# Performance work log

Measured on AMD Instinct MI355X. Metric: run time of the kernel, lower is better.

## Reference

```python
import jax, jax.numpy as jnp
import numpy as np

D_MODEL = 2048
N_HEADS = 16
HEAD_DIM = D_MODEL // N_HEADS  # 128
B, T = 2, 2048


def setup_inputs() -> dict:
    key = jax.random.key(0)
    ks = jax.random.split(key, 5)
    s = 0.02
    x = jax.random.normal(ks[0], (B, T, D_MODEL), dtype=jnp.float32)
    # weights stored as [in, out] (math-equivalent to torch Linear's W.T)
    Wq = jax.random.normal(ks[1], (D_MODEL, D_MODEL), dtype=jnp.float32) * s
    Wk = jax.random.normal(ks[2], (D_MODEL, HEAD_DIM), dtype=jnp.float32) * s
    Wv = jax.random.normal(ks[3], (D_MODEL, HEAD_DIM), dtype=jnp.float32) * s
    Wo = jax.random.normal(ks[4], (D_MODEL, D_MODEL), dtype=jnp.float32) * s
    return {"x": x, "Wq": Wq, "Wk": Wk, "Wv": Wv, "Wo": Wo}


def reference(x, Wq, Wk, Wv, Wo):
    Bx, Tx, Dx = x.shape
    scale = HEAD_DIM ** -0.5
    # q: (B, H, T, hd); k, v: single shared head (B, T, hd)
    q = (x @ Wq).reshape(Bx, Tx, N_HEADS, HEAD_DIM).transpose(0, 2, 1, 3)
    k = x @ Wk  # (B, T, hd)
    v = x @ Wv  # (B, T, hd)
    # scores: (B, H, T, T) -- shared KV head broadcast across query heads
    attn = jnp.einsum('bhqd,bkd->bhqk', q, k) * scale
    causal = jnp.triu(jnp.ones((Tx, Tx), dtype=bool), k=1)  # True = masked
    attn = jnp.where(causal[None, None], -jnp.inf, attn)
    weights = jax.nn.softmax(attn, axis=-1)
    weights = jnp.nan_to_num(weights)
    out = jnp.einsum('bhqk,bkd->bhqd', weights, v)  # (B, H, T, hd)
    out = out.transpose(0, 2, 1, 3).reshape(Bx, Tx, Dx)
    return out @ Wo
```

## Files before the change

### kernel.cpp

```cpp
#include <hip/hip_runtime.h>

typedef __bf16 bf16x8 __attribute__((ext_vector_type(8)));
typedef float f32x4 __attribute__((ext_vector_type(4)));

__device__ inline void gload16(const __bf16* g, __bf16* l) {
  __builtin_amdgcn_global_load_lds(
      (const __attribute__((address_space(1))) unsigned int*)g,
      (__attribute__((address_space(3))) unsigned int*)l, 16, 0, 0);
}

__global__ __launch_bounds__(256) void conv_bf16(
    const float* __restrict__ in, __bf16* __restrict__ out)
{
  size_t i = ((size_t)blockIdx.x * 256 + threadIdx.x) * 8;
  float4 a = *(const float4*)&in[i];
  float4 b = *(const float4*)&in[i + 4];
  bf16x8 h;
  h[0] = (__bf16)a.x; h[1] = (__bf16)a.y; h[2] = (__bf16)a.z; h[3] = (__bf16)a.w;
  h[4] = (__bf16)b.x; h[5] = (__bf16)b.y; h[6] = (__bf16)b.z; h[7] = (__bf16)b.w;
  *(bf16x8*)&out[i] = h;
}

__global__ __launch_bounds__(256) void transpose_w(
    const float* __restrict__ W, __bf16* __restrict__ WT, int Kd, int Nd)
{
  __shared__ __bf16 Ts[64 * 72];
  const int tid = threadIdx.x;
  const int c0 = blockIdx.x * 64, r0 = blockIdx.y * 64;
#pragma unroll
  for (int i = 0; i < 4; i++) {
    int row = (tid >> 4) + i * 16, cv = (tid & 15) * 4;
    float4 w = *(const float4*)&W[(size_t)(r0 + row) * Nd + c0 + cv];
    Ts[(cv + 0) * 72 + row] = (__bf16)w.x;
    Ts[(cv + 1) * 72 + row] = (__bf16)w.y;
    Ts[(cv + 2) * 72 + row] = (__bf16)w.z;
    Ts[(cv + 3) * 72 + row] = (__bf16)w.w;
  }
  __syncthreads();
#pragma unroll
  for (int i = 0; i < 4; i++) {
    int n = (tid >> 4) + i * 16, kseg = (tid & 15) * 4;
    *(uint2*)&WT[(size_t)(c0 + n) * Kd + r0 + kseg] = *(uint2*)&Ts[n * 72 + kseg];
  }
}

__global__ __launch_bounds__(256) void gemm_qkv(
    const __bf16* __restrict__ A, const __bf16* __restrict__ WqT,
    const __bf16* __restrict__ WkT, const __bf16* __restrict__ WvT,
    __bf16* __restrict__ Cq, __bf16* __restrict__ Ck, __bf16* __restrict__ Cv)
{
  __shared__ __align__(16) __bf16 Asl[128 * 32];
  __shared__ __align__(16) __bf16 Bsl[128 * 32];
  const int tid = threadIdx.x, wave = tid >> 6, lane = tid & 63;
  const int quad = lane >> 4, l16 = lane & 15;
  const int nb = blockIdx.x, m0 = blockIdx.y * 128;
  const __bf16* BT; __bf16* C; int ldC, c0;
  if (nb < 16)       { BT = WqT + (size_t)nb * 128 * 2048; C = Cq; ldC = 2048; c0 = nb * 128; }
  else if (nb == 16) { BT = WkT; C = Ck; ldC = 128; c0 = 0; }
  else               { BT = WvT; C = Cv; ldC = 128; c0 = 0; }
  const int wm = (wave >> 1) * 64, wn = (wave & 1) * 64;
  const int lrow = lane >> 2, lseg = (lane & 3) * 8;

  f32x4 acc[4][4];
#pragma unroll
  for (int i = 0; i < 4; i++)
#pragma unroll
    for (int j = 0; j < 4; j++) acc[i][j] = (f32x4){0.f, 0.f, 0.f, 0.f};

  for (int k0 = 0; k0 < 2048; k0 += 32) {
    __syncthreads();
#pragma unroll
    for (int c = 0; c < 2; c++) {
      int ch = wave * 2 + c;
      gload16(&A[(size_t)(m0 + ch * 16 + lrow) * 2048 + k0 + lseg], &Asl[ch * 512]);
      gload16(&BT[(size_t)(ch * 16 + lrow) * 2048 + k0 + lseg], &Bsl[ch * 512]);
    }
    __syncthreads();

    bf16x8 af[4], bf[4];
#pragma unroll
    for (int i = 0; i < 4; i++)
      af[i] = *(const bf16x8*)&Asl[(wm + i * 16 + l16) * 32 + quad * 8];
#pragma unroll
    for (int i = 0; i < 4; i++)
      bf[i] = *(const bf16x8*)&Bsl[(wn + i * 16 + l16) * 32 + quad * 8];
#pragma unroll
    for (int mi = 0; mi < 4; mi++)
#pragma unroll
      for (int ni = 0; ni < 4; ni++)
        acc[mi][ni] = __builtin_amdgcn_mfma_f32_16x16x32_bf16(
            af[mi], bf[ni], acc[mi][ni], 0, 0, 0);
  }

#pragma unroll
  for (int mi = 0; mi < 4; mi++)
#pragma unroll
    for (int ni = 0; ni < 4; ni++)
#pragma unroll
      for (int r = 0; r < 4; r++) {
        int row = m0 + wm + mi * 16 + quad * 4 + r;
        int col = c0 + wn + ni * 16 + l16;
        C[(size_t)row * ldC + col] = (__bf16)acc[mi][ni][r];
      }
}

__global__ __launch_bounds__(256) void gemm_out_bt(
    const __bf16* __restrict__ A, const __bf16* __restrict__ BT,
    float* __restrict__ Cp)
{
  __shared__ __align__(16) __bf16 Asl[128 * 32];
  __shared__ __align__(16) __bf16 Bsl[128 * 32];
  const int tid = threadIdx.x, wave = tid >> 6, lane = tid & 63;
  const int quad = lane >> 4, l16 = lane & 15;
  const int n0 = blockIdx.x * 128, m0 = blockIdx.y * 128;
  const int wm = (wave >> 1) * 64, wn = (wave & 1) * 64;
  const int lrow = lane >> 2, lseg = (lane & 3) * 8;

  f32x4 acc[4][4];
#pragma unroll
  for (int i = 0; i < 4; i++)
#pragma unroll
    for (int j = 0; j < 4; j++) acc[i][j] = (f32x4){0.f, 0.f, 0.f, 0.f};

  for (int k0 = 0; k0 < 2048; k0 += 32) {
    __syncthreads();
#pragma unroll
    for (int c = 0; c < 2; c++) {
      int ch = wave * 2 + c;
      gload16(&A[(size_t)(m0 + ch * 16 + lrow) * 2048 + k0 + lseg], &Asl[ch * 512]);
      gload16(&BT[(size_t)(n0 + ch * 16 + lrow) * 2048 + k0 + lseg], &Bsl[ch * 512]);
    }
    __syncthreads();

    bf16x8 af[4], bf[4];
#pragma unroll
    for (int i = 0; i < 4; i++)
      af[i] = *(const bf16x8*)&Asl[(wm + i * 16 + l16) * 32 + quad * 8];
#pragma unroll
    for (int i = 0; i < 4; i++)
      bf[i] = *(const bf16x8*)&Bsl[(wn + i * 16 + l16) * 32 + quad * 8];
#pragma unroll
    for (int mi = 0; mi < 4; mi++)
#pragma unroll
      for (int ni = 0; ni < 4; ni++)
        acc[mi][ni] = __builtin_amdgcn_mfma_f32_16x16x32_bf16(
            af[mi], bf[ni], acc[mi][ni], 0, 0, 0);
  }

#pragma unroll
  for (int mi = 0; mi < 4; mi++)
#pragma unroll
    for (int ni = 0; ni < 4; ni++)
#pragma unroll
      for (int r = 0; r < 4; r++) {
        int row = m0 + wm + mi * 16 + quad * 4 + r;
        int col = n0 + wn + ni * 16 + l16;
        Cp[(size_t)row * 2048 + col] = acc[mi][ni][r];
      }
}

__global__ __launch_bounds__(256) void gemm_out_f32b(
    const __bf16* __restrict__ A, const float* __restrict__ B,
    float* __restrict__ Cp)
{
  __shared__ __align__(16) __bf16 Asl[128 * 32];
  __shared__ __align__(16) __bf16 BsT[128 * 32];
  const int tid = threadIdx.x, wave = tid >> 6, lane = tid & 63;
  const int quad = lane >> 4, l16 = lane & 15;
  const int n0 = blockIdx.x * 128, m0 = blockIdx.y * 128;
  const int wm = (wave >> 1) * 64, wn = (wave & 1) * 64;
  const int lrow = lane >> 2, lseg = (lane & 3) * 8;
  const int kg = (tid >> 5) * 4, ng = (tid & 31) * 4;

  f32x4 acc[4][4];
#pragma unroll
  for (int i = 0; i < 4; i++)
#pragma unroll
    for (int j = 0; j < 4; j++) acc[i][j] = (f32x4){0.f, 0.f, 0.f, 0.f};

  for (int k0 = 0; k0 < 2048; k0 += 32) {
    __syncthreads();
#pragma unroll
    for (int c = 0; c < 2; c++) {
      int ch = wave * 2 + c;
      gload16(&A[(size_t)(m0 + ch * 16 + lrow) * 2048 + k0 + lseg], &Asl[ch * 512]);
    }
    __bf16 h[4][4];
#pragma unroll
    for (int i = 0; i < 4; i++) {
      float4 w = *(const float4*)&B[(size_t)(k0 + kg + i) * 2048 + n0 + ng];
      h[i][0] = (__bf16)w.x; h[i][1] = (__bf16)w.y;
      h[i][2] = (__bf16)w.z; h[i][3] = (__bf16)w.w;
    }
#pragma unroll
    for (int j = 0; j < 4; j++) {
      int n = ng + j;
      int pb = ((kg >> 3) + (n >> 2)) & 3;
      __bf16 o4[4] = {h[0][j], h[1][j], h[2][j], h[3][j]};
      *(uint2*)&BsT[n * 32 + pb * 8 + (kg & 7)] = *(uint2*)o4;
    }
    __syncthreads();

    bf16x8 af[4], bf[4];
#pragma unroll
    for (int i = 0; i < 4; i++)
      af[i] = *(const bf16x8*)&Asl[(wm + i * 16 + l16) * 32 + quad * 8];
#pragma unroll
    for (int i = 0; i < 4; i++) {
      int n = wn + i * 16 + l16;
      int pb = (quad + (n >> 2)) & 3;
      bf[i] = *(const bf16x8*)&BsT[n * 32 + pb * 8];
    }
#pragma unroll
    for (int mi = 0; mi < 4; mi++)
#pragma unroll
      for (int ni = 0; ni < 4; ni++)
        acc[mi][ni] = __builtin_amdgcn_mfma_f32_16x16x32_bf16(
            af[mi], bf[ni], acc[mi][ni], 0, 0, 0);
  }

#pragma unroll
  for (int mi = 0; mi < 4; mi++)
#pragma unroll
    for (int ni = 0; ni < 4; ni++)
#pragma unroll
      for (int r = 0; r < 4; r++) {
        int row = m0 + wm + mi * 16 + quad * 4 + r;
        int col = n0 + wn + ni * 16 + l16;
        Cp[(size_t)row * 2048 + col] = acc[mi][ni][r];
      }
}

#define KS_LD 136
#define VT_LD 72
#define PR_LD 72

__global__ __launch_bounds__(256) void mqa_attn_mfma(
    const __bf16* Q, const __bf16* __restrict__ Km,
    const __bf16* __restrict__ Vm, __bf16* O)
{
  __shared__ __align__(16) __bf16 Ks[64 * KS_LD];
  __shared__ __align__(16) __bf16 VsT[128 * VT_LD];
  __shared__ __align__(16) __bf16 Pr[4][32 * PR_LD];

  const int tid = threadIdx.x, wave = tid >> 6, lane = tid & 63;
  const int quad = lane >> 4, l16 = lane & 15;
  const int t = blockIdx.x >> 1, bat = blockIdx.x & 1;
  const int hg = blockIdx.y & 3, flip = blockIdx.y >> 2;
  const int qt = flip ? (63 - t) : t;
  const int h = hg * 4 + wave;
  const int q0 = qt * 32;
  const size_t qgrow = (size_t)bat * 2048 + q0;
  const float SCL2 = 0.08838834764831845f * 1.4426950408889634f;

  bf16x8 qf[2][4];
#pragma unroll
  for (int mi = 0; mi < 2; mi++)
#pragma unroll
    for (int ks = 0; ks < 4; ks++)
      qf[mi][ks] = *(const bf16x8*)(Q + (qgrow + mi * 16 + l16) * 2048 +
                                    h * 128 + ks * 32 + quad * 8);

  bf16x8 ones;
#pragma unroll
  for (int i = 0; i < 8; i++) ones[i] = (__bf16)1.0f;

  f32x4 oa[2][8];
#pragma unroll
  for (int mi = 0; mi < 2; mi++)
#pragma unroll
    for (int nt = 0; nt < 8; nt++) oa[mi][nt] = (f32x4){0.f, 0.f, 0.f, 0.f};
  f32x4 lacc[2];
  lacc[0] = (f32x4){0.f, 0.f, 0.f, 0.f};
  lacc[1] = (f32x4){0.f, 0.f, 0.f, 0.f};

  const __bf16* Kb = Km + (size_t)bat * 2048 * 128;
  const __bf16* Vb = Vm + (size_t)bat * 2048 * 128;
  const int qmax = q0 + 31;

  for (int sc = 0; sc <= qmax; sc += 64) {
    __syncthreads();
#pragma unroll
    for (int i = 0; i < 4; i++) {
      int v = tid + i * 256;
      int row = v >> 4, dseg = (v & 15) * 8;
      int kr = sc + row; if (kr > 2047) kr = 2047;
      *(bf16x8*)&Ks[row * KS_LD + dseg] =
          *(const bf16x8*)&Kb[(size_t)kr * 128 + dseg];
    }
#pragma unroll
    for (int i = 0; i < 2; i++) {
      int g = tid + i * 256;
      int dg = (g & 31) * 4, kg2 = (g >> 5) * 4;
      union { uint2 u; unsigned short s[4]; } a[4], o;
#pragma unroll
      for (int i2 = 0; i2 < 4; i2++) {
        int kr = sc + kg2 + i2; if (kr > 2047) kr = 2047;
        a[i2].u = *(const uint2*)&Vb[(size_t)kr * 128 + dg];
      }
#pragma unroll
      for (int j = 0; j < 4; j++) {
        int d = dg + j;
        int pb = ((kg2 >> 3) + (d >> 2)) & 7;
        o.s[0] = a[0].s[j]; o.s[1] = a[1].s[j];
        o.s[2] = a[2].s[j]; o.s[3] = a[3].s[j];
        *(uint2*)&VsT[d * VT_LD + pb * 8 + (kg2 & 7)] = o.u;
      }
    }
    __syncthreads();

    f32x4 sf[2][4];
#pragma unroll
    for (int mi = 0; mi < 2; mi++)
#pragma unroll
      for (int kt = 0; kt < 4; kt++) sf[mi][kt] = (f32x4){0.f, 0.f, 0.f, 0.f};
#pragma unroll
    for (int ks = 0; ks < 4; ks++)
#pragma unroll
      for (int kt = 0; kt < 4; kt++) {
        bf16x8 kf = *(const bf16x8*)&Ks[(kt * 16 + l16) * KS_LD + ks * 32 + quad * 8];
        sf[0][kt] = __builtin_amdgcn_mfma_f32_16x16x32_bf16(kf, qf[0][ks], sf[0][kt], 0, 0, 0);
        sf[1][kt] = __builtin_amdgcn_mfma_f32_16x16x32_bf16(kf, qf[1][ks], sf[1][kt], 0, 0, 0);
      }

    __bf16* prw = Pr[wave];
    if (sc + 64 > q0) {
#pragma unroll
      for (int mi = 0; mi < 2; mi++) {
        int qrow = q0 + mi * 16 + l16;
#pragma unroll
        for (int kt = 0; kt < 4; kt++) {
          int kbase = sc + kt * 16 + quad * 4;
          __bf16 h4[4];
#pragma unroll
          for (int r = 0; r < 4; r++) {
            float p = (kbase + r <= qrow) ? exp2f(sf[mi][kt][r] * SCL2) : 0.f;
            h4[r] = (__bf16)p;
          }
          *(uint2*)&prw[(mi * 16 + l16) * PR_LD + kt * 16 + quad * 4] = *(uint2*)h4;
        }
      }
    } else {
#pragma unroll
      for (int mi = 0; mi < 2; mi++)
#pragma unroll
        for (int kt = 0; kt < 4; kt++) {
          __bf16 h4[4];
#pragma unroll
          for (int r = 0; r < 4; r++) h4[r] = (__bf16)exp2f(sf[mi][kt][r] * SCL2);
          *(uint2*)&prw[(mi * 16 + l16) * PR_LD + kt * 16 + quad * 4] = *(uint2*)h4;
        }
    }

#pragma unroll
    for (int ks2 = 0; ks2 < 2; ks2++) {
      bf16x8 pf0 = *(const bf16x8*)&prw[(l16) * PR_LD + ks2 * 32 + quad * 8];
      bf16x8 pf1 = *(const bf16x8*)&prw[(16 + l16) * PR_LD + ks2 * 32 + quad * 8];
      lacc[0] = __builtin_amdgcn_mfma_f32_16x16x32_bf16(pf0, ones, lacc[0], 0, 0, 0);
      lacc[1] = __builtin_amdgcn_mfma_f32_16x16x32_bf16(pf1, ones, lacc[1], 0, 0, 0);
#pragma unroll
      for (int nt = 0; nt < 8; nt++) {
        int d = nt * 16 + l16;
        int pb = ((ks2 * 4 + quad) + (d >> 2)) & 7;
        bf16x8 vf = *(const bf16x8*)&VsT[d * VT_LD + pb * 8];
        oa[0][nt] = __builtin_amdgcn_mfma_f32_16x16x32_bf16(pf0, vf, oa[0][nt], 0, 0, 0);
        oa[1][nt] = __builtin_amdgcn_mfma_f32_16x16x32_bf16(pf1, vf, oa[1][nt], 0, 0, 0);
      }
    }
  }

#pragma unroll
  for (int mi = 0; mi < 2; mi++)
#pragma unroll
    for (int r = 0; r < 4; r++) {
      float inv = 1.f / lacc[mi][r];
      size_t row = qgrow + mi * 16 + quad * 4 + r;
#pragma unroll
      for (int nt = 0; nt < 8; nt++)
        O[row * 2048 + h * 128 + nt * 16 + l16] = (__bf16)(oa[mi][nt][r] * inv);
    }
}

extern "C" void kernel_launch(void* const* d_in, const int* in_sizes, int n_in,
                              void* d_out, int out_size, void* d_ws, size_t ws_size,
                              hipStream_t stream) {
  const float* x  = (const float*)d_in[0];
  const float* Wq = (const float*)d_in[1];
  const float* Wk = (const float*)d_in[2];
  const float* Wv = (const float*)d_in[3];
  const float* Wo = (const float*)d_in[4];
  float* out = (float*)d_out;

  __bf16* q   = (__bf16*)d_ws;
  __bf16* WoT = (__bf16*)((char*)d_ws + 16777216);
  const bool have_wot = ws_size >= (size_t)(16777216 + 8388608);

  char* ob = (char*)d_out;
  __bf16* xb  = (__bf16*)(ob);
  __bf16* WqT = (__bf16*)(ob + 16777216);
  __bf16* WkT = (__bf16*)(ob + 25165824);
  __bf16* WvT = (__bf16*)(ob + 25690112);
  __bf16* kb  = (__bf16*)(ob + 26214400);
  __bf16* vb  = (__bf16*)(ob + 27262976);

  dim3 blk(256);
  conv_bf16<<<4096, blk, 0, stream>>>(x, xb);
  transpose_w<<<dim3(32, 32), blk, 0, stream>>>(Wq, WqT, 2048, 2048);
  transpose_w<<<dim3(2, 32), blk, 0, stream>>>(Wk, WkT, 2048, 128);
  transpose_w<<<dim3(2, 32), blk, 0, stream>>>(Wv, WvT, 2048, 128);
  if (have_wot)
    transpose_w<<<dim3(32, 32), blk, 0, stream>>>(Wo, WoT, 2048, 2048);
  gemm_qkv<<<dim3(18, 32), blk, 0, stream>>>(xb, WqT, WkT, WvT, q, kb, vb);
  mqa_attn_mfma<<<dim3(64, 8, 1), blk, 0, stream>>>(q, kb, vb, q);
  if (have_wot)
    gemm_out_bt<<<dim3(16, 32), blk, 0, stream>>>(q, WoT, out);
  else
    gemm_out_f32b<<<dim3(16, 32), blk, 0, stream>>>(q, Wo, out);
}
```

Baseline: 299.4 us.

## Use direct-to-LDS loads for attention K/V via pre-transposed V, and double the GEMM K-step

After: 307.6 us. 1.03x slower.

```diff
diff --git a/kernel.cpp b/kernel.cpp
--- a/kernel.cpp
+++ b/kernel.cpp
@@ -44,13 +44,38 @@
   }
 }
 
+__global__ __launch_bounds__(256) void transpose_v(
+    const __bf16* __restrict__ V, __bf16* __restrict__ VT)
+{
+  __shared__ __bf16 Ts[64 * 72];
+  const int tid = threadIdx.x;
+  const int t0 = blockIdx.x * 64, d0 = blockIdx.y * 64, bz = blockIdx.z;
+#pragma unroll
+  for (int i = 0; i < 4; i++) {
+    int tr = (tid >> 4) + i * 16, dc = (tid & 15) * 4;
+    union { uint2 u; __bf16 h[4]; } v;
+    v.u = *(const uint2*)&V[(size_t)(bz * 2048 + t0 + tr) * 128 + d0 + dc];
+    Ts[(dc + 0) * 72 + tr] = v.h[0];
+    Ts[(dc + 1) * 72 + tr] = v.h[1];
+    Ts[(dc + 2) * 72 + tr] = v.h[2];
+    Ts[(dc + 3) * 72 + tr] = v.h[3];
+  }
+  __syncthreads();
+#pragma unroll
+  for (int i = 0; i < 4; i++) {
+    int d = (tid >> 4) + i * 16, ts = (tid & 15) * 4;
+    *(uint2*)&VT[(size_t)bz * 128 * 2048 + (size_t)(d0 + d) * 2048 + t0 + ts] =
+        *(uint2*)&Ts[d * 72 + ts];
+  }
+}
+
 __global__ __launch_bounds__(256) void gemm_qkv(
     const __bf16* __restrict__ A, const __bf16* __restrict__ WqT,
     const __bf16* __restrict__ WkT, const __bf16* __restrict__ WvT,
     __bf16* __restrict__ Cq, __bf16* __restrict__ Ck, __bf16* __restrict__ Cv)
 {
-  __shared__ __align__(16) __bf16 Asl[128 * 32];
-  __shared__ __align__(16) __bf16 Bsl[128 * 32];
+  __shared__ __align__(16) __bf16 Apan[2][128 * 32];
+  __shared__ __align__(16) __bf16 Bpan[2][128 * 32];
   const int tid = threadIdx.x, wave = tid >> 6, lane = tid & 63;
   const int quad = lane >> 4, l16 = lane & 15;
   const int nb = blockIdx.x, m0 = blockIdx.y * 128;
@@ -59,7 +84,7 @@
   else if (nb == 16) { BT = WkT; C = Ck; ldC = 128; c0 = 0; }
   else               { BT = WvT; C = Cv; ldC = 128; c0 = 0; }
   const int wm = (wave >> 1) * 64, wn = (wave & 1) * 64;
-  const int lrow = lane >> 2, lseg = (lane & 3) * 8;
+  const int srow = lane >> 2, sseg = (lane & 3) * 8;
 
   f32x4 acc[4][4];
 #pragma unroll
@@ -67,29 +92,33 @@
 #pragma unroll
     for (int j = 0; j < 4; j++) acc[i][j] = (f32x4){0.f, 0.f, 0.f, 0.f};
 
-  for (int k0 = 0; k0 < 2048; k0 += 32) {
-    __syncthreads();
-#pragma unroll
-    for (int c = 0; c < 2; c++) {
-      int ch = wave * 2 + c;
-      gload16(&A[(size_t)(m0 + ch * 16 + lrow) * 2048 + k0 + lseg], &Asl[ch * 512]);
-      gload16(&BT[(size_t)(ch * 16 + lrow) * 2048 + k0 + lseg], &Bsl[ch * 512]);
-    }
-    __syncthreads();
-
-    bf16x8 af[4], bf[4];
-#pragma unroll
-    for (int i = 0; i < 4; i++)
-      af[i] = *(const bf16x8*)&Asl[(wm + i * 16 + l16) * 32 + quad * 8];
-#pragma unroll
-    for (int i = 0; i < 4; i++)
-      bf[i] = *(const bf16x8*)&Bsl[(wn + i * 16 + l16) * 32 + quad * 8];
-#pragma unroll
-    for (int mi = 0; mi < 4; mi++)
-#pragma unroll
-      for (int ni = 0; ni < 4; ni++)
-        acc[mi][ni] = __builtin_amdgcn_mfma_f32_16x16x32_bf16(
-            af[mi], bf[ni], acc[mi][ni], 0, 0, 0);
+  for (int k0 = 0; k0 < 2048; k0 += 64) {
+    __syncthreads();
+#pragma unroll
+    for (int c = 0; c < 4; c++) {
+      int idx = wave * 4 + c;
+      int p = idx >> 3, rg = (idx & 7) * 16;
+      gload16(&A[(size_t)(m0 + rg + srow) * 2048 + k0 + p * 32 + sseg], &Apan[p][rg * 32]);
+      gload16(&BT[(size_t)(rg + srow) * 2048 + k0 + p * 32 + sseg], &Bpan[p][rg * 32]);
+    }
+    __syncthreads();
+
+#pragma unroll
+    for (int ks = 0; ks < 2; ks++) {
+      bf16x8 af[4], bf[4];
+#pragma unroll
+      for (int i = 0; i < 4; i++)
+        af[i] = *(const bf16x8*)&Apan[ks][(wm + i * 16 + l16) * 32 + quad * 8];
+#pragma unroll
+      for (int i = 0; i < 4; i++)
+        bf[i] = *(const bf16x8*)&Bpan[ks][(wn + i * 16 + l16) * 32 + quad * 8];
+#pragma unroll
+      for (int mi = 0; mi < 4; mi++)
+#pragma unroll
+        for (int ni = 0; ni < 4; ni++)
+          acc[mi][ni] = __builtin_amdgcn_mfma_f32_16x16x32_bf16(
+              af[mi], bf[ni], acc[mi][ni], 0, 0, 0);
+    }
   }
 
 #pragma unroll
@@ -108,13 +137,13 @@
     const __bf16* __restrict__ A, const __bf16* __restrict__ BT,
     float* __restrict__ Cp)
 {
-  __shared__ __align__(16) __bf16 Asl[128 * 32];
-  __shared__ __align__(16) __bf16 Bsl[128 * 32];
+  __shared__ __align__(16) __bf16 Apan[2][128 * 32];
+  __shared__ __align__(16) __bf16 Bpan[2][128 * 32];
   const int tid = threadIdx.x, wave = tid >> 6, lane = tid & 63;
   const int quad = lane >> 4, l16 = lane & 15;
   const int n0 = blockIdx.x * 128, m0 = blockIdx.y * 128;
   const int wm = (wave >> 1) * 64, wn = (wave & 1) * 64;
-  const int lrow = lane >> 2, lseg = (lane & 3) * 8;
+  const int srow = lane >> 2, sseg = (lane & 3) * 8;
 
   f32x4 acc[4][4];
 #pragma unroll
@@ -122,29 +151,33 @@
 #pragma unroll
     for (int j = 0; j < 4; j++) acc[i][j] = (f32x4){0.f, 0.f, 0.f, 0.f};
 
-  for (int k0 = 0; k0 < 2048; k0 += 32) {
-    __syncthreads();
-#pragma unroll
-    for (int c = 0; c < 2; c++) {
-      int ch = wave * 2 + c;
-      gload16(&A[(size_t)(m0 + ch * 16 + lrow) * 2048 + k0 + lseg], &Asl[ch * 512]);
-      gload16(&BT[(size_t)(n0 + ch * 16 + lrow) * 2048 + k0 + lseg], &Bsl[ch * 512]);
-    }
-    __syncthreads();
-
-    bf16x8 af[4], bf[4];
-#pragma unroll
-    for (int i = 0; i < 4; i++)
-      af[i] = *(const bf16x8*)&Asl[(wm + i * 16 + l16) * 32 + quad * 8];
-#pragma unroll
-    for (int i = 0; i < 4; i++)
-      bf[i] = *(const bf16x8*)&Bsl[(wn + i * 16 + l16) * 32 + quad * 8];
-#pragma unroll
-    for (int mi = 0; mi < 4; mi++)
-#pragma unroll
-      for (int ni = 0; ni < 4; ni++)
-        acc[mi][ni] = __builtin_amdgcn_mfma_f32_16x16x32_bf16(
-            af[mi], bf[ni], acc[mi][ni], 0, 0, 0);
+  for (int k0 = 0; k0 < 2048; k0 += 64) {
+    __syncthreads();
+#pragma unroll
+    for (int c = 0; c < 4; c++) {
+      int idx = wave * 4 + c;
+      int p = idx >> 3, rg = (idx & 7) * 16;
+      gload16(&A[(size_t)(m0 + rg + srow) * 2048 + k0 + p * 32 + sseg], &Apan[p][rg * 32]);
+      gload16(&BT[(size_t)(n0 + rg + srow) * 2048 + k0 + p * 32 + sseg], &Bpan[p][rg * 32]);
+    }
+    __syncthreads();
+
+#pragma unroll
+    for (int ks = 0; ks < 2; ks++) {
+      bf16x8 af[4], bf[4];
+#pragma unroll
+      for (int i = 0; i < 4; i++)
+        af[i] = *(const bf16x8*)&Apan[ks][(wm + i * 16 + l16) * 32 + quad * 8];
+#pragma unroll
+      for (int i = 0; i < 4; i++)
+        bf[i] = *(const bf16x8*)&Bpan[ks][(wn + i * 16 + l16) * 32 + quad * 8];
+#pragma unroll
+      for (int mi = 0; mi < 4; mi++)
+#pragma unroll
+        for (int ni = 0; ni < 4; ni++)
+          acc[mi][ni] = __builtin_amdgcn_mfma_f32_16x16x32_bf16(
+              af[mi], bf[ni], acc[mi][ni], 0, 0, 0);
+    }
   }
 
 #pragma unroll
@@ -231,16 +264,14 @@
       }
 }
 
-#define KS_LD 136
-#define VT_LD 72
 #define PR_LD 72
 
 __global__ __launch_bounds__(256) void mqa_attn_mfma(
     const __bf16* Q, const __bf16* __restrict__ Km,
-    const __bf16* __restrict__ Vm, __bf16* O)
-{
-  __shared__ __align__(16) __bf16 Ks[64 * KS_LD];
-  __shared__ __align__(16) __bf16 VsT[128 * VT_LD];
+    const __bf16* __restrict__ VTm, __bf16* O)
+{
+  __shared__ __align__(16) __bf16 KsP[4][64 * 32];
+  __shared__ __align__(16) __bf16 VsP[2][128 * 32];
   __shared__ __align__(16) __bf16 Pr[4][32 * PR_LD];
 
   const int tid = threadIdx.x, wave = tid >> 6, lane = tid & 63;
@@ -274,38 +305,23 @@
   lacc[0] = (f32x4){0.f, 0.f, 0.f, 0.f};
   lacc[1] = (f32x4){0.f, 0.f, 0.f, 0.f};
 
-  const __bf16* Kb = Km + (size_t)bat * 2048 * 128;
-  const __bf16* Vb = Vm + (size_t)bat * 2048 * 128;
+  const __bf16* Kb  = Km  + (size_t)bat * 2048 * 128;
+  const __bf16* VTb = VTm + (size_t)bat * 128 * 2048;
   const int qmax = q0 + 31;
+  const int srow = lane >> 2, sseg = (lane & 3) * 8;
+  const int vp = wave >> 1, vdb = (wave & 1) * 64;
 
   for (int sc = 0; sc <= qmax; sc += 64) {
     __syncthreads();
 #pragma unroll
-    for (int i = 0; i < 4; i++) {
-      int v = tid + i * 256;
-      int row = v >> 4, dseg = (v & 15) * 8;
-      int kr = sc + row; if (kr > 2047) kr = 2047;
-      *(bf16x8*)&Ks[row * KS_LD + dseg] =
-          *(const bf16x8*)&Kb[(size_t)kr * 128 + dseg];
-    }
-#pragma unroll
-    for (int i = 0; i < 2; i++) {
-      int g = tid + i * 256;
-      int dg = (g & 31) * 4, kg2 = (g >> 5) * 4;
-      union { uint2 u; unsigned short s[4]; } a[4], o;
-#pragma unroll
-      for (int i2 = 0; i2 < 4; i2++) {
-        int kr = sc + kg2 + i2; if (kr > 2047) kr = 2047;
-        a[i2].u = *(const uint2*)&Vb[(size_t)kr * 128 + dg];
-      }
-#pragma unroll
-      for (int j = 0; j < 4; j++) {
-        int d = dg + j;
-        int pb = ((kg2 >> 3) + (d >> 2)) & 7;
-        o.s[0] = a[0].s[j]; o.s[1] = a[1].s[j];
-        o.s[2] = a[2].s[j]; o.s[3] = a[3].s[j];
-        *(uint2*)&VsT[d * VT_LD + pb * 8 + (kg2 & 7)] = o.u;
-      }
+    for (int c = 0; c < 4; c++) {
+      int kr = sc + c * 16 + srow; if (kr > 2047) kr = 2047;
+      gload16(&Kb[(size_t)kr * 128 + wave * 32 + sseg], &KsP[wave][c * 512]);
+    }
+#pragma unroll
+    for (int c = 0; c < 4; c++) {
+      int d = vdb + c * 16 + srow;
+      gload16(&VTb[(size_t)d * 2048 + sc + vp * 32 + sseg], &VsP[vp][(vdb + c * 16) * 32]);
     }
     __syncthreads();
 
@@ -318,7 +334,7 @@
     for (int ks = 0; ks < 4; ks++)
 #pragma unroll
       for (int kt = 0; kt < 4; kt++) {
-        bf16x8 kf = *(const bf16x8*)&Ks[(kt * 16 + l16) * KS_LD + ks * 32 + quad * 8];
+        bf16x8 kf = *(const bf16x8*)&KsP[ks][(kt * 16 + l16) * 32 + quad * 8];
         sf[0][kt] = __builtin_amdgcn_mfma_f32_16x16x32_bf16(kf, qf[0][ks], sf[0][kt], 0, 0, 0);
         sf[1][kt] = __builtin_amdgcn_mfma_f32_16x16x32_bf16(kf, qf[1][ks], sf[1][kt], 0, 0, 0);
       }
@@ -360,9 +376,7 @@
       lacc[1] = __builtin_amdgcn_mfma_f32_16x16x32_bf16(pf1, ones, lacc[1], 0, 0, 0);
 #pragma unroll
       for (int nt = 0; nt < 8; nt++) {
-        int d = nt * 16 + l16;
-        int pb = ((ks2 * 4 + quad) + (d >> 2)) & 7;
-        bf16x8 vf = *(const bf16x8*)&VsT[d * VT_LD + pb * 8];
+        bf16x8 vf = *(const bf16x8*)&VsP[ks2][(nt * 16 + l16) * 32 + quad * 8];
         oa[0][nt] = __builtin_amdgcn_mfma_f32_16x16x32_bf16(pf0, vf, oa[0][nt], 0, 0, 0);
         oa[1][nt] = __builtin_amdgcn_mfma_f32_16x16x32_bf16(pf1, vf, oa[1][nt], 0, 0, 0);
       }
@@ -402,6 +416,7 @@
   __bf16* WvT = (__bf16*)(ob + 25690112);
   __bf16* kb  = (__bf16*)(ob + 26214400);
   __bf16* vb  = (__bf16*)(ob + 27262976);
+  __bf16* vT  = (__bf16*)(ob + 28311552);
 
   dim3 blk(256);
   conv_bf16<<<4096, blk, 0, stream>>>(x, xb);
@@ -411,7 +426,8 @@
   if (have_wot)
     transpose_w<<<dim3(32, 32), blk, 0, stream>>>(Wo, WoT, 2048, 2048);
   gemm_qkv<<<dim3(18, 32), blk, 0, stream>>>(xb, WqT, WkT, WvT, q, kb, vb);
-  mqa_attn_mfma<<<dim3(64, 8, 1), blk, 0, stream>>>(q, kb, vb, q);
+  transpose_v<<<dim3(32, 2, 2), blk, 0, stream>>>(vb, vT);
+  mqa_attn_mfma<<<dim3(64, 8, 1), blk, 0, stream>>>(q, kb, vT, q);
   if (have_wot)
     gemm_out_bt<<<dim3(16, 32), blk, 0, stream>>>(q, WoT, out);
   else
```
